# Kernel tuning notes

Hardware: AMD Instinct MI355X
Metric: run time of the kernel (lower is better)

## Reference

```python
import jax, jax.numpy as jnp
import numpy as np

OUT, GROUPS, GRID = 4096, 1, 8   # 2^bits = 8 -> 3-bit codes
IN = 4096
B, S = 4, 2048

def setup_inputs() -> dict:
    key = jax.random.key(0)
    k1, k2, k3 = jax.random.split(key, 3)
    x = jax.random.normal(k1, (B, S, IN), dtype=jnp.float32)
    quant_grid = jax.random.normal(k2, (OUT, GROUPS, GRID), dtype=jnp.float32) * 0.02
    weight_codes = jax.random.randint(k3, (OUT, GROUPS, IN // GROUPS), 0, GRID, dtype=jnp.int32)
    return {"x": x, "quant_grid": quant_grid, "weight_codes": weight_codes}

def reference(x, quant_grid, weight_codes):
    # Dequantize: per-(row, group) codebook lookup -> full weight [OUT, IN]
    W = jnp.take_along_axis(quant_grid, weight_codes, axis=-1)  # [OUT, GROUPS, IN//GROUPS]
    W = W.reshape(W.shape[0], -1)                               # [OUT, IN]
    # y = X @ W.T
    return jnp.einsum('bsi,oi->bso', x, W)
```

## Files before the change

### kernel.cpp

```cpp
#include <hip/hip_runtime.h>


#define M_DIM 8192
#define N_DIM 4096
#define K_DIM 4096
#define BK 64
#define NKT (K_DIM / BK)

typedef __attribute__((ext_vector_type(4))) int int32x4;

#define AS1 __attribute__((address_space(1)))
#define AS3 __attribute__((address_space(3)))

__device__ __forceinline__ void gl_lds16(const void* g, void* l) {
    __builtin_amdgcn_global_load_lds((const AS1 void*)g, (AS3 void*)l, 16, 0, 0);
}

__global__ __launch_bounds__(256) void quant_x(const float* __restrict__ X,
                                               char* __restrict__ XQ,
                                               float* __restrict__ SX) {
    const int row = blockIdx.x;
    const int t = threadIdx.x;
    const float4* xp = (const float4*)(X + (size_t)row * K_DIM);
    float4 v[4];
    float mx = 0.0f;
#pragma unroll
    for (int i = 0; i < 4; ++i) {
        v[i] = xp[t * 4 + i];
        mx = fmaxf(mx, fmaxf(fmaxf(fabsf(v[i].x), fabsf(v[i].y)),
                             fmaxf(fabsf(v[i].z), fabsf(v[i].w))));
    }
#pragma unroll
    for (int off = 1; off < 64; off <<= 1)
        mx = fmaxf(mx, __shfl_xor(mx, off));
    __shared__ float wmx[4];
    if ((t & 63) == 0) wmx[t >> 6] = mx;
    __syncthreads();
    mx = fmaxf(fmaxf(wmx[0], wmx[1]), fmaxf(wmx[2], wmx[3]));
    const float inv = 127.0f / mx;
    int4 o4;
    int* po = (int*)&o4;
#pragma unroll
    for (int i = 0; i < 4; ++i) {
        int q0 = (int)rintf(v[i].x * inv);
        int q1 = (int)rintf(v[i].y * inv);
        int q2 = (int)rintf(v[i].z * inv);
        int q3 = (int)rintf(v[i].w * inv);
        po[i] = (q0 & 255) | ((q1 & 255) << 8) | ((q2 & 255) << 16) | ((q3 & 255) << 24);
    }
    ((int4*)(XQ + (size_t)row * K_DIM))[t] = o4;
    if (t == 0) SX[row] = mx * (1.0f / 127.0f);
}

__global__ __launch_bounds__(256) void quant_w(const int* __restrict__ CD,
                                               const float* __restrict__ G,
                                               char* __restrict__ WQ,
                                               float* __restrict__ SW) {
    const int o = blockIdx.x;
    __shared__ int gq[8];
    if (threadIdx.x == 0) {
        float g[8], mx = 0.0f;
#pragma unroll
        for (int j = 0; j < 8; ++j) { g[j] = G[o * 8 + j]; mx = fmaxf(mx, fabsf(g[j])); }
        mx = fmaxf(mx, 1e-20f);
        const float inv = 127.0f / mx;
        SW[o] = mx * (1.0f / 127.0f);
#pragma unroll
        for (int j = 0; j < 8; ++j) gq[j] = ((int)rintf(g[j] * inv)) & 255;
    }
    __syncthreads();
    const int4* cp = (const int4*)(CD + (size_t)o * K_DIM);
    int* wp = (int*)(WQ + (size_t)o * K_DIM);
#pragma unroll
    for (int r = 0; r < 4; ++r) {
        int idx = r * 256 + threadIdx.x;
        int4 c = cp[idx];
        wp[idx] = gq[c.x] | (gq[c.y] << 8) | (gq[c.z] << 16) | (gq[c.w] << 24);
    }
}

__global__ __launch_bounds__(256, 2) void gemm3(const char* __restrict__ A,
                                                const char* __restrict__ B,
                                                const float* __restrict__ SX,
                                                const float* __restrict__ SW,
                                                float* __restrict__ C) {
    __shared__ char As[3][256 * 64];
    __shared__ char Bs[3][128 * 64];

    const int tid = threadIdx.x;
    const int lane = tid & 63;
    const int wid = tid >> 6;
    const int wm = wid >> 1;
    const int wn = wid & 1;

    int wg = blockIdx.x;
    wg = (wg & 7) * (gridDim.x >> 3) + (wg >> 3);
    const int ntn = N_DIM / 128;
    const int bm = (wg / ntn) * 256;
    const int bn = (wg % ntn) * 128;

    const int fr = lane & 15;
    const int g = lane >> 4;
    const int offk = fr * 64 + ((g ^ ((fr >> 1) & 3)) << 4);
    const int awoff = wm * 8192;
    const int bwoff = wn * 4096;

    const int row0 = tid >> 2;
    const int sl = (((tid & 3) ^ ((row0 >> 1) & 3)) << 4);
    const char* gA0 = A + (size_t)(bm + row0) * K_DIM + sl;
    const char* gA1 = A + (size_t)(bm + 64 + row0) * K_DIM + sl;
    const char* gA2 = A + (size_t)(bm + 128 + row0) * K_DIM + sl;
    const char* gA3 = A + (size_t)(bm + 192 + row0) * K_DIM + sl;
    const char* gB0 = B + (size_t)(bn + row0) * K_DIM + sl;
    const char* gB1 = B + (size_t)(bn + 64 + row0) * K_DIM + sl;

#define KCL(KT) (((KT) < NKT) ? (KT) : 0)

#define STG(BUF, KT) do {                                                          \
        const int kb_ = KCL(KT) * BK;                                              \
        gl_lds16(gA0 + kb_, &As[BUF][0] + tid * 16);                               \
        gl_lds16(gA1 + kb_, &As[BUF][4096] + tid * 16);                            \
        gl_lds16(gA2 + kb_, &As[BUF][8192] + tid * 16);                            \
        gl_lds16(gA3 + kb_, &As[BUF][12288] + tid * 16);                           \
        gl_lds16(gB0 + kb_, &Bs[BUF][0] + tid * 16);                               \
        gl_lds16(gB1 + kb_, &Bs[BUF][4096] + tid * 16);                            \
    } while (0)

#define RD_B(CUR)                                                                  \
    _Pragma("unroll") for (int n = 0; n < 4; ++n)                                  \
        fb[n] = *(const int32x4*)&Bs[CUR][bwoff + n * 1024 + offk];

#define RD_A(CUR)                                                                  \
    _Pragma("unroll") for (int m = 0; m < 8; ++m)                                  \
        fa[m] = *(const int32x4*)&As[CUR][awoff + m * 1024 + offk];

#define MF_ALL                                                                     \
    _Pragma("unroll") for (int m = 0; m < 8; ++m)                                  \
    _Pragma("unroll") for (int n = 0; n < 4; ++n)                                  \
        acc[m][n] = __builtin_amdgcn_mfma_i32_16x16x64_i8(fa[m], fb[n], acc[m][n], 0, 0, 0);

#define BODY(CUR, NXT2, T) do {                                                    \
        STG(NXT2, (T) + 2);                                                        \
        RD_B(CUR) RD_A(CUR)                                                        \
        __builtin_amdgcn_s_setprio(1);                                             \
        MF_ALL                                                                     \
        __builtin_amdgcn_s_setprio(0);                                             \
        __builtin_amdgcn_sched_barrier(0);                                         \
        asm volatile("s_waitcnt vmcnt(6)" ::: "memory");                           \
        __builtin_amdgcn_s_barrier();                                              \
    } while (0)

    int32x4 acc[8][4] = {};
    int32x4 fa[8];
    int32x4 fb[4];

    STG(0, 0);
    STG(1, 1);
    asm volatile("s_waitcnt vmcnt(6)" ::: "memory");
    __builtin_amdgcn_s_barrier();

    for (int j = 0; j < 21; ++j) {
        const int t = 3 * j;
        BODY(0, 2, t);
        BODY(1, 0, t + 1);
        BODY(2, 1, t + 2);
    }
    BODY(0, 2, 63);
    asm volatile("s_waitcnt vmcnt(0)" ::: "memory");

    const int crow0 = bm + wm * 128 + (g << 2);
    const int ccol0 = bn + wn * 64 + fr;
    float swc[4];
#pragma unroll
    for (int ni = 0; ni < 4; ++ni) swc[ni] = SW[ccol0 + ni * 16];
#pragma unroll
    for (int mi = 0; mi < 8; ++mi)
#pragma unroll
        for (int r = 0; r < 4; ++r) {
            const float sxr = SX[crow0 + mi * 16 + r];
#pragma unroll
            for (int ni = 0; ni < 4; ++ni)
                C[(size_t)(crow0 + mi * 16 + r) * N_DIM + ccol0 + ni * 16] =
                    (float)acc[mi][ni][r] * sxr * swc[ni];
        }
}

__global__ __launch_bounds__(256) void fb_gemm(const float* __restrict__ X,
                                               const float* __restrict__ G,
                                               const int* __restrict__ CD,
                                               float* __restrict__ Y) {
    __shared__ float xs[16][64];
    __shared__ float ws[16][64];
    const int bm = blockIdx.y << 6, bn = blockIdx.x << 6;
    const int tid = threadIdx.x;
    const int tn = tid & 15, tm = tid >> 4;
    float acc[4][4] = {};
    for (int k0 = 0; k0 < K_DIM; k0 += 16) {
#pragma unroll
        for (int r = 0; r < 4; ++r) {
            int e = r * 256 + tid;
            int mm = e >> 4, kk = e & 15;
            xs[kk][mm] = X[(size_t)(bm + mm) * K_DIM + k0 + kk];
            int code = CD[(size_t)(bn + mm) * K_DIM + k0 + kk];
            ws[kk][mm] = G[(bn + mm) * 8 + code];
        }
        __syncthreads();
#pragma unroll
        for (int kk = 0; kk < 16; ++kk)
#pragma unroll
            for (int i = 0; i < 4; ++i)
#pragma unroll
                for (int j = 0; j < 4; ++j)
                    acc[i][j] += xs[kk][tm * 4 + i] * ws[kk][tn * 4 + j];
        __syncthreads();
    }
#pragma unroll
    for (int i = 0; i < 4; ++i)
#pragma unroll
        for (int j = 0; j < 4; ++j)
            Y[(size_t)(bm + tm * 4 + i) * N_DIM + bn + tn * 4 + j] = acc[i][j];
}

extern "C" void kernel_launch(void* const* d_in, const int* in_sizes, int n_in,
                              void* d_out, int out_size, void* d_ws, size_t ws_size,
                              hipStream_t stream) {
    const float* x = (const float*)d_in[0];
    const float* qg = (const float*)d_in[1];
    const int* wc = (const int*)d_in[2];
    float* y = (float*)d_out;

    const size_t sx_off = 0;
    const size_t sw_off = (size_t)M_DIM * 4;
    const size_t xq_off = (size_t)(M_DIM + N_DIM) * 4;
    const size_t wq_off = xq_off + (size_t)M_DIM * K_DIM;
    const size_t need = wq_off + (size_t)N_DIM * K_DIM;

    if (ws_size >= need) {
        float* sx = (float*)((char*)d_ws + sx_off);
        float* sw = (float*)((char*)d_ws + sw_off);
        char* xq = (char*)d_ws + xq_off;
        char* wq = (char*)d_ws + wq_off;
        hipLaunchKernelGGL(quant_x, dim3(M_DIM), dim3(256), 0, stream, x, xq, sx);
        hipLaunchKernelGGL(quant_w, dim3(N_DIM), dim3(256), 0, stream, wc, qg, wq, sw);
        const int nwg = (M_DIM / 256) * (N_DIM / 128);
        hipLaunchKernelGGL(gemm3, dim3(nwg), dim3(256), 0, stream,
                           xq, wq, sx, sw, y);
    } else {
        hipLaunchKernelGGL(fb_gemm, dim3(N_DIM / 64, M_DIM / 64), dim3(256), 0, stream,
                           x, qg, wc, y);
    }
}
```

Baseline: 205.2 us.

## Enlarge int8 GEMM tile to 256x256 with 8 waves and paired-tile pipeline

Switches the int8 MFMA GEMM from 256x128 tiles with 4 waves to 256x256 tiles with 512 threads (8 waves, 2x4 wave grid). This raises data reuse per loaded byte. LDS grows to four 32KB stages. The main loop now stages two k-tiles, computes two, then does a full vmcnt(0) wait and a barrier, which halves the number of barriers. The costs are 128KB of LDS per block, which limits residency to one block per CU, a coarser wait that may expose load latency, and fewer workgroups in the grid.

```diff
diff --git a/kernel.cpp b/kernel.cpp
--- a/kernel.cpp
+++ b/kernel.cpp
@@ -79,25 +79,25 @@
     }
 }
 
-__global__ __launch_bounds__(256, 2) void gemm3(const char* __restrict__ A,
+__global__ __launch_bounds__(512, 2) void gemm4(const char* __restrict__ A,
                                                 const char* __restrict__ B,
                                                 const float* __restrict__ SX,
                                                 const float* __restrict__ SW,
                                                 float* __restrict__ C) {
-    __shared__ char As[3][256 * 64];
-    __shared__ char Bs[3][128 * 64];
+    __shared__ char As[4][256 * 64];
+    __shared__ char Bs[4][256 * 64];
 
     const int tid = threadIdx.x;
     const int lane = tid & 63;
     const int wid = tid >> 6;
-    const int wm = wid >> 1;
-    const int wn = wid & 1;
+    const int wm = wid >> 2;
+    const int wn = wid & 3;
 
     int wg = blockIdx.x;
     wg = (wg & 7) * (gridDim.x >> 3) + (wg >> 3);
-    const int ntn = N_DIM / 128;
+    const int ntn = N_DIM / 256;
     const int bm = (wg / ntn) * 256;
-    const int bn = (wg % ntn) * 128;
+    const int bn = (wg % ntn) * 256;
 
     const int fr = lane & 15;
     const int g = lane >> 4;
@@ -108,47 +108,44 @@
     const int row0 = tid >> 2;
     const int sl = (((tid & 3) ^ ((row0 >> 1) & 3)) << 4);
     const char* gA0 = A + (size_t)(bm + row0) * K_DIM + sl;
-    const char* gA1 = A + (size_t)(bm + 64 + row0) * K_DIM + sl;
-    const char* gA2 = A + (size_t)(bm + 128 + row0) * K_DIM + sl;
-    const char* gA3 = A + (size_t)(bm + 192 + row0) * K_DIM + sl;
+    const char* gA1 = A + (size_t)(bm + 128 + row0) * K_DIM + sl;
     const char* gB0 = B + (size_t)(bn + row0) * K_DIM + sl;
-    const char* gB1 = B + (size_t)(bn + 64 + row0) * K_DIM + sl;
+    const char* gB1 = B + (size_t)(bn + 128 + row0) * K_DIM + sl;
 
 #define KCL(KT) (((KT) < NKT) ? (KT) : 0)
 
 #define STG(BUF, KT) do {                                                          \
         const int kb_ = KCL(KT) * BK;                                              \
-        gl_lds16(gA0 + kb_, &As[BUF][0] + tid * 16);                               \
-        gl_lds16(gA1 + kb_, &As[BUF][4096] + tid * 16);                            \
-        gl_lds16(gA2 + kb_, &As[BUF][8192] + tid * 16);                            \
-        gl_lds16(gA3 + kb_, &As[BUF][12288] + tid * 16);                           \
-        gl_lds16(gB0 + kb_, &Bs[BUF][0] + tid * 16);                               \
-        gl_lds16(gB1 + kb_, &Bs[BUF][4096] + tid * 16);                            \
+        gl_lds16(gA0 + kb_, &As[BUF][0] + wid * 1024);                             \
+        gl_lds16(gA1 + kb_, &As[BUF][8192] + wid * 1024);                          \
+        gl_lds16(gB0 + kb_, &Bs[BUF][0] + wid * 1024);                             \
+        gl_lds16(gB1 + kb_, &Bs[BUF][8192] + wid * 1024);                          \
     } while (0)
 
-#define RD_B(CUR)                                                                  \
+#define RD_B(BUF)                                                                  \
     _Pragma("unroll") for (int n = 0; n < 4; ++n)                                  \
-        fb[n] = *(const int32x4*)&Bs[CUR][bwoff + n * 1024 + offk];
-
-#define RD_A(CUR)                                                                  \
+        fb[n] = *(const int32x4*)&Bs[BUF][bwoff + n * 1024 + offk];
+
+#define RD_A(BUF)                                                                  \
     _Pragma("unroll") for (int m = 0; m < 8; ++m)                                  \
-        fa[m] = *(const int32x4*)&As[CUR][awoff + m * 1024 + offk];
+        fa[m] = *(const int32x4*)&As[BUF][awoff + m * 1024 + offk];
 
 #define MF_ALL                                                                     \
     _Pragma("unroll") for (int m = 0; m < 8; ++m)                                  \
     _Pragma("unroll") for (int n = 0; n < 4; ++n)                                  \
         acc[m][n] = __builtin_amdgcn_mfma_i32_16x16x64_i8(fa[m], fb[n], acc[m][n], 0, 0, 0);
 
-#define BODY(CUR, NXT2, T) do {                                                    \
-        STG(NXT2, (T) + 2);                                                        \
-        RD_B(CUR) RD_A(CUR)                                                        \
+#define TILE(BUF) do {                                                             \
+        RD_B(BUF) RD_A(BUF)                                                        \
         __builtin_amdgcn_s_setprio(1);                                             \
         MF_ALL                                                                     \
         __builtin_amdgcn_s_setprio(0);                                             \
         __builtin_amdgcn_sched_barrier(0);                                         \
-        asm volatile("s_waitcnt vmcnt(6)" ::: "memory");                           \
-        __builtin_amdgcn_s_barrier();                                              \
     } while (0)
+
+#define PAIR_END                                                                   \
+    asm volatile("s_waitcnt vmcnt(0)" ::: "memory");                               \
+    __builtin_amdgcn_s_barrier();
 
     int32x4 acc[8][4] = {};
     int32x4 fa[8];
@@ -156,17 +153,21 @@
 
     STG(0, 0);
     STG(1, 1);
-    asm volatile("s_waitcnt vmcnt(6)" ::: "memory");
-    __builtin_amdgcn_s_barrier();
-
-    for (int j = 0; j < 21; ++j) {
-        const int t = 3 * j;
-        BODY(0, 2, t);
-        BODY(1, 0, t + 1);
-        BODY(2, 1, t + 2);
-    }
-    BODY(0, 2, 63);
-    asm volatile("s_waitcnt vmcnt(0)" ::: "memory");
+    PAIR_END
+
+    for (int jj = 0; jj < 16; ++jj) {
+        const int t0 = 4 * jj;
+        STG(2, t0 + 2);
+        STG(3, t0 + 3);
+        TILE(0);
+        TILE(1);
+        PAIR_END
+        STG(0, t0 + 4);
+        STG(1, t0 + 5);
+        TILE(2);
+        TILE(3);
+        PAIR_END
+    }
 
     const int crow0 = bm + wm * 128 + (g << 2);
     const int ccol0 = bn + wn * 64 + fr;
@@ -242,8 +243,8 @@
         char* wq = (char*)d_ws + wq_off;
         hipLaunchKernelGGL(quant_x, dim3(M_DIM), dim3(256), 0, stream, x, xq, sx);
         hipLaunchKernelGGL(quant_w, dim3(N_DIM), dim3(256), 0, stream, wc, qg, wq, sw);
-        const int nwg = (M_DIM / 256) * (N_DIM / 128);
-        hipLaunchKernelGGL(gemm3, dim3(nwg), dim3(256), 0, stream,
+        const int nwg = (M_DIM / 256) * (N_DIM / 256);
+        hipLaunchKernelGGL(gemm4, dim3(nwg), dim3(512), 0, stream,
                            xq, wq, sx, sw, y);
     } else {
         hipLaunchKernelGGL(fb_gemm, dim3(N_DIM / 64, M_DIM / 64), dim3(256), 0, stream,
```

Result: faster. 198.3 us (-3.4%).
